# Performance work log

Measured on AMD Instinct MI355X. Metric: run time of the kernel, lower is better.

Reference implementation:

```python
import jax, jax.numpy as jnp
import numpy as np

T, E = 16384, 1024   # frames, feature dim (WavLM-Large)
M, K = 8, 512        # number of kmeans models, clusters per model


def setup_inputs() -> dict:
    key = jax.random.key(0)
    k1, k2, k3 = jax.random.split(key, 3)
    emb = jax.random.normal(k1, (1, T, E), dtype=jnp.float32)
    centroids = jax.random.normal(k2, (M, K, E), dtype=jnp.float32)
    # per-frame random kmeans model choice (stride=1): replaces random.randint in the loop
    model_idx = jax.random.randint(k3, (T,), 0, M, dtype=jnp.int32)
    return {"emb": emb, "centroids": centroids, "model_idx": model_idx}


def reference(emb, centroids, model_idx):
    # emb: [1,T,E], centroids: [M,K,E], model_idx: [T] in [0,M)
    x = emb[0]  # [T,E]
    # squared euclidean distance from every frame to every centroid of every model
    # (argmin over squared dist == argmin over cdist)
    x_sq = jnp.sum(x * x, axis=-1)                      # [T]
    c_sq = jnp.sum(centroids * centroids, axis=-1)      # [M,K]
    dots = jnp.einsum('te,mke->tmk', x, centroids)      # [T,M,K]
    d_all = x_sq[:, None, None] - 2.0 * dots + c_sq[None, :, :]  # [T,M,K]
    # select the randomly chosen model's distances per frame
    d = jnp.take_along_axis(d_all, model_idx[:, None, None].astype(jnp.int32), axis=1)[:, 0, :]  # [T,K]
    codes = jnp.argmin(d, axis=-1)                      # [T]
    # embedding lookup: the quantizer's emb maps cluster id -> centroid vector
    out = centroids[model_idx, codes]                   # [T,E]
    return out[None]  # [1,T,E]
```

## Files before the change

kernel.cpp:

```cpp
#include <hip/hip_runtime.h>


#define T_FRAMES 16384
#define E_DIM    1024
#define M_MODELS 8
#define K_CLUST  512

#define FPB  64
#define NCH  8
#define CHG  16

typedef __bf16 bf16x8 __attribute__((ext_vector_type(8)));
typedef float  floatx16 __attribute__((ext_vector_type(16)));

__device__ __forceinline__ bf16x8 cvt8(const float4 a, const float4 b) {
  bf16x8 h;
  h[0] = (__bf16)a.x; h[1] = (__bf16)a.y; h[2] = (__bf16)a.z; h[3] = (__bf16)a.w;
  h[4] = (__bf16)b.x; h[5] = (__bf16)b.y; h[6] = (__bf16)b.z; h[7] = (__bf16)b.w;
  return h;
}

__global__ __launch_bounds__(256) void k_csq(const float* __restrict__ cent,
                                             double* __restrict__ csq64) {
  const int row = blockIdx.x * 4 + (threadIdx.x >> 6);
  const int lane = threadIdx.x & 63;
  const float* p = cent + (size_t)row * E_DIM;
  double s = 0.0;
#pragma unroll
  for (int i = 0; i < 16; ++i) {
    const float v = p[lane + i * 64];
    s += (double)v * (double)v;
  }
#pragma unroll
  for (int m = 32; m >= 1; m >>= 1) s += __shfl_xor(s, m, 64);
  if (lane == 0) csq64[row] = s;
}

__global__ __launch_bounds__(256) void k_cvt(const float* __restrict__ cent,
                                             float* __restrict__ out) {
  const int b = blockIdx.x;
  const int m = b >> 6;
  const int cg = (b >> 2) & 15;
  const int q = b & 3;
  const int tid = threadIdx.x;
  const int ci = tid & 31;
  const int gk0 = q * 32 + (tid >> 5) * 4;
  const int B32 = (m * 16 + cg) * 32;
  const float* src = cent + ((size_t)(m * K_CLUST + cg * 32 + ci)) * E_DIM;
#pragma unroll
  for (int j = 0; j < 4; ++j) {
    const int gk = gk0 + j;
    const float4 a = *(const float4*)(src + gk * 8);
    const float4 bb = *(const float4*)(src + gk * 8 + 4);
    const size_t foff = (size_t)(B32 + (gk >> 2)) * 1024 + 512 +
                        ((gk & 3) * 32 + ci) * 4;
    *(bf16x8*)(out + foff) = cvt8(a, bb);
  }
}

__global__ __launch_bounds__(256) void k_hist(const int* __restrict__ midx,
                                              int* __restrict__ hist) {
  __shared__ int h[M_MODELS * 33];
  const int tid = threadIdx.x;
  for (int i = tid; i < M_MODELS * 33; i += 256) h[i] = 0;
  __syncthreads();
  const int m = midx[blockIdx.x * 256 + tid];
  atomicAdd(&h[m * 33 + (tid & 31)], 1);
  __syncthreads();
  if (tid < M_MODELS) {
    int s = 0;
    for (int j = 0; j < 32; ++j) s += h[tid * 33 + j];
    hist[blockIdx.x * M_MODELS + tid] = s;
  }
}

__global__ __launch_bounds__(256) void k_scatter(const int* __restrict__ midx,
                                                 const int* __restrict__ hist,
                                                 int* __restrict__ order,
                                                 int* __restrict__ offs) {
  __shared__ int h2[64 * M_MODELS];
  __shared__ int cur[M_MODELS];
  const int tid = threadIdx.x;
  h2[tid] = hist[tid];
  h2[tid + 256] = hist[tid + 256];
  __syncthreads();
  if (tid < M_MODELS) {
    int tot_before = 0;
    for (int mp = 0; mp < tid; ++mp)
      for (int b = 0; b < 64; ++b) tot_before += h2[b * M_MODELS + mp];
    int prior = 0;
    for (int b = 0; b < (int)blockIdx.x; ++b) prior += h2[b * M_MODELS + tid];
    cur[tid] = tot_before + prior;
  }
  if (blockIdx.x == 0 && tid <= M_MODELS) {
    int o = 0;
    for (int mp = 0; mp < tid; ++mp)
      for (int b = 0; b < 64; ++b) o += h2[b * M_MODELS + mp];
    offs[tid] = o;
  }
  __syncthreads();
  const int f = blockIdx.x * 256 + tid;
  const int pos = atomicAdd(&cur[midx[f]], 1);
  order[pos] = f;
}

__global__ __launch_bounds__(256, 1) void k_dist(const float* __restrict__ emb,
                                                 const double* __restrict__ csq64,
                                                 const int* __restrict__ order,
                                                 const int* __restrict__ offs,
                                                 float* __restrict__ out) {
  const int m = blockIdx.x;
  const int o0 = offs[m];
  const int cnt = offs[m + 1] - o0;
  const int start = blockIdx.y * FPB;
  if (start >= cnt) return;
  const int nvalid = min(FPB, cnt - start);

  __shared__ __align__(16) __bf16 A_l[2 * CHG * FPB * 8];

  const int tid = threadIdx.x;
  const int l = tid & 63;
  const int w = tid >> 6;
  const int ln = l & 31;
  const int lh = l >> 5;

  const int s_row = tid >> 2;
  const int s_g = (tid & 3) * 4;
  const size_t arow4 = (size_t)order[o0 + start + min(s_row, nvalid - 1)] * (E_DIM / 4);
  const float4* emb4 = (const float4*)emb;

  float4 pa[8];
#pragma unroll
  for (int j = 0; j < 4; ++j) {
    pa[2 * j] = emb4[arow4 + (s_g + j) * 2];
    pa[2 * j + 1] = emb4[arow4 + (s_g + j) * 2 + 1];
  }
#pragma unroll
  for (int j = 0; j < 4; ++j)
    *(bf16x8*)(A_l + ((size_t)(s_g + j) * FPB + s_row) * 8) = cvt8(pa[2 * j], pa[2 * j + 1]);

  const char* bbase[4];
#pragma unroll
  for (int ct = 0; ct < 4; ++ct) {
    const int cg = w * 4 + ct;
    bbase[ct] = (const char*)out + (size_t)(m * 16 + cg) * 131072 + 2048 + l * 16;
  }
#define LOADB(ct, kb) (*(const bf16x8*)(bbase[ct] + (((kb) >> 1) << 12) + (((kb) & 1) << 10)))

  bf16x8 bR[2][4];
#pragma unroll
  for (int ct = 0; ct < 4; ++ct) {
    bR[0][ct] = LOADB(ct, 0);
    bR[1][ct] = LOADB(ct, 1);
  }

  floatx16 acc[8] = {};
  __syncthreads();

  for (int c = 0; c < NCH; ++c) {
    const int buf = (c & 1) * CHG;
    if (c + 1 < NCH) {
#pragma unroll
      for (int j = 0; j < 4; ++j) {
        pa[2 * j] = emb4[arow4 + (c + 1) * 32 + (s_g + j) * 2];
        pa[2 * j + 1] = emb4[arow4 + (c + 1) * 32 + (s_g + j) * 2 + 1];
      }
    }
#pragma unroll
    for (int jj = 0; jj < 8; ++jj) {
      const int kb = c * 8 + jj;
      const int p = jj & 1;
      const bf16x8 a0 = *(const bf16x8*)(A_l + ((size_t)(buf + jj * 2 + lh) * FPB + ln) * 8);
      const bf16x8 a1 = *(const bf16x8*)(A_l + ((size_t)(buf + jj * 2 + lh) * FPB + 32 + ln) * 8);
#pragma unroll
      for (int ct = 0; ct < 4; ++ct) {
        acc[ct] = __builtin_amdgcn_mfma_f32_32x32x16_bf16(a0, bR[p][ct], acc[ct], 0, 0, 0);
        acc[4 + ct] = __builtin_amdgcn_mfma_f32_32x32x16_bf16(a1, bR[p][ct], acc[4 + ct], 0, 0, 0);
      }
      if (kb + 2 < 64) {
#pragma unroll
        for (int ct = 0; ct < 4; ++ct) bR[p][ct] = LOADB(ct, kb + 2);
      }
    }
    __syncthreads();
    if (c + 1 < NCH) {
      const int nbuf = ((c + 1) & 1) * CHG;
#pragma unroll
      for (int j = 0; j < 4; ++j)
        *(bf16x8*)(A_l + ((size_t)(nbuf + s_g + j) * FPB + s_row) * 8) = cvt8(pa[2 * j], pa[2 * j + 1]);
      __syncthreads();
    }
  }

#pragma unroll
  for (int ct = 0; ct < 4; ++ct) {
    const int col = w * 128 + ct * 32 + ln;
    const float cs = (float)csq64[m * K_CLUST + col];
#pragma unroll
    for (int rt = 0; rt < 2; ++rt) {
#pragma unroll
      for (int r = 0; r < 16; ++r) {
        const int frow = rt * 32 + (r & 3) + 8 * (r >> 2) + 4 * lh;
        const int t = order[o0 + start + min(frow, nvalid - 1)];
        out[(size_t)t * E_DIM + col] = cs - 2.0f * acc[rt * 4 + ct][r];
      }
    }
  }
#undef LOADB
}

__global__ __launch_bounds__(256) void k_pick(const float* __restrict__ emb,
                                              const float* __restrict__ cent,
                                              const double* __restrict__ csq64,
                                              const int* __restrict__ midx,
                                              float* __restrict__ out) {
  const int t = blockIdx.x * 4 + (threadIdx.x >> 6);
  const int l = threadIdx.x & 63;
  const int m = midx[t];

  const float4* orow4 = (const float4*)(out + (size_t)t * E_DIM);
  const float4 v0 = orow4[l * 2];
  const float4 v1 = orow4[l * 2 + 1];
  float sv[8] = {v0.x, v0.y, v0.z, v0.w, v1.x, v1.y, v1.z, v1.w};

  float bm = sv[0];
  int bc = l * 8;
#pragma unroll
  for (int j = 1; j < 8; ++j)
    if (sv[j] < bm) { bm = sv[j]; bc = l * 8 + j; }
#pragma unroll
  for (int s = 32; s >= 1; s >>= 1) {
    const float om = __shfl_xor(bm, s, 64);
    const int oc = __shfl_xor(bc, s, 64);
    if (om < bm || (om == bm && oc < bc)) { bm = om; bc = oc; }
  }

  const float thr = bm + 3.0f;
  unsigned long long bal[8];
  int ncand = 0;
#pragma unroll
  for (int j = 0; j < 8; ++j) {
    bal[j] = __ballot(sv[j] < thr);
    ncand += __popcll(bal[j]);
  }

  int best = bc;
  if (ncand > 1) {
    float4 xv[4];
#pragma unroll
    for (int q = 0; q < 4; ++q)
      xv[q] = *(const float4*)(emb + (size_t)t * E_DIM + q * 256 + l * 4);
    double bd = 1e300;
    int bi = 1 << 30;
#pragma unroll
    for (int j = 0; j < 8; ++j) {
      unsigned long long mb = bal[j];
      while (mb) {
        const int L = __ffsll(mb) - 1;
        mb &= mb - 1;
        const int c = L * 8 + j;
        const float* crow = cent + ((size_t)m * K_CLUST + c) * E_DIM;
        double s = 0.0;
#pragma unroll
        for (int q = 0; q < 4; ++q) {
          const float4 cv = *(const float4*)(crow + q * 256 + l * 4);
          s += (double)xv[q].x * (double)cv.x + (double)xv[q].y * (double)cv.y +
               (double)xv[q].z * (double)cv.z + (double)xv[q].w * (double)cv.w;
        }
#pragma unroll
        for (int sh = 32; sh >= 1; sh >>= 1) s += __shfl_xor(s, sh, 64);
        const double d = csq64[m * K_CLUST + c] - 2.0 * s;
        if (d < bd || (d == bd && c < bi)) { bd = d; bi = c; }
      }
    }
    best = bi;
  }

  const float* crow = cent + ((size_t)m * K_CLUST + best) * E_DIM;
  float* drow = out + (size_t)t * E_DIM;
#pragma unroll
  for (int q = 0; q < 4; ++q)
    *(float4*)(drow + q * 256 + l * 4) = *(const float4*)(crow + q * 256 + l * 4);
}

extern "C" void kernel_launch(void* const* d_in, const int* in_sizes, int n_in,
                              void* d_out, int out_size, void* d_ws, size_t ws_size,
                              hipStream_t stream) {
  const float* emb = (const float*)d_in[0];
  const float* cent = (const float*)d_in[1];
  const int* midx = (const int*)d_in[2];
  float* out = (float*)d_out;

  char* ws = (char*)d_ws;
  double* csq64 = (double*)(ws + 0);
  int* hist = (int*)(ws + 32768);
  int* offs = (int*)(ws + 34816);
  int* order = (int*)(ws + 34880);

  hipLaunchKernelGGL(k_csq, dim3(1024), dim3(256), 0, stream, cent, csq64);
  hipLaunchKernelGGL(k_cvt, dim3(512), dim3(256), 0, stream, cent, out);
  hipLaunchKernelGGL(k_hist, dim3(64), dim3(256), 0, stream, midx, hist);
  hipLaunchKernelGGL(k_scatter, dim3(64), dim3(256), 0, stream, midx, hist, order, offs);
  hipLaunchKernelGGL(k_dist, dim3(M_MODELS, 40), dim3(256), 0, stream,
                     emb, csq64, order, offs, out);
  hipLaunchKernelGGL(k_pick, dim3(T_FRAMES / 4), dim3(256), 0, stream,
                     emb, cent, csq64, midx, out);
}
```

Baseline: 208.6 us.

## Fuse argmin and fp64 candidate refinement into distance kernel, shrink frame tile

The distance GEMM kernel now computes the per-frame argmin directly from MFMA accumulators, using wave shuffles and shared memory. Candidates within the threshold are collected in shared memory and refined in fp64 inside the same kernel. Only an int code per frame is written, so the full fp32 distance matrix no longer makes a round trip through global memory. The frame tile drops from 64 to 32 with two blocks per CU and twice the grid, and a new lightweight gather kernel copies the centroid rows. The risks are halved reuse of each B fragment per frame and the candidate cap of 32 per frame in shared memory.

```diff
diff --git a/kernel.cpp b/kernel.cpp
--- a/kernel.cpp
+++ b/kernel.cpp
@@ -6,9 +6,8 @@
 #define M_MODELS 8
 #define K_CLUST  512
 
-#define FPB  64
-#define NCH  8
-#define CHG  16
+#define FPB 32
+#define NCH 8
 
 typedef __bf16 bf16x8 __attribute__((ext_vector_type(8)));
 typedef float  floatx16 __attribute__((ext_vector_type(16)));
@@ -104,7 +103,8 @@
   order[pos] = f;
 }
 
-__global__ __launch_bounds__(256, 1) void k_dist(const float* __restrict__ emb,
+__global__ __launch_bounds__(256, 2) void k_dist(const float* __restrict__ emb,
+                                                 const float* __restrict__ cent,
                                                  const double* __restrict__ csq64,
                                                  const int* __restrict__ order,
                                                  const int* __restrict__ offs,
@@ -116,7 +116,13 @@
   if (start >= cnt) return;
   const int nvalid = min(FPB, cnt - start);
 
-  __shared__ __align__(16) __bf16 A_l[2 * CHG * FPB * 8];
+  __shared__ __align__(16) __bf16 A_l[2 * 16 * FPB * 8];
+  __shared__ int rows_l[FPB];
+  __shared__ float wmin_s[4][FPB];
+  __shared__ int wcol_s[4][FPB];
+  __shared__ float gmin_s[FPB];
+  __shared__ int cnt_s[FPB];
+  __shared__ int cand_s[FPB][32];
 
   const int tid = threadIdx.x;
   const int l = tid & 63;
@@ -124,20 +130,19 @@
   const int ln = l & 31;
   const int lh = l >> 5;
 
-  const int s_row = tid >> 2;
-  const int s_g = (tid & 3) * 4;
-  const size_t arow4 = (size_t)order[o0 + start + min(s_row, nvalid - 1)] * (E_DIM / 4);
+  if (tid < FPB) rows_l[tid] = order[o0 + start + min(tid, nvalid - 1)];
+  __syncthreads();
+
+  const int s_row = tid & 31;
+  const int s_gp = tid >> 5;
   const float4* emb4 = (const float4*)emb;
-
-  float4 pa[8];
-#pragma unroll
-  for (int j = 0; j < 4; ++j) {
-    pa[2 * j] = emb4[arow4 + (s_g + j) * 2];
-    pa[2 * j + 1] = emb4[arow4 + (s_g + j) * 2 + 1];
-  }
-#pragma unroll
-  for (int j = 0; j < 4; ++j)
-    *(bf16x8*)(A_l + ((size_t)(s_g + j) * FPB + s_row) * 8) = cvt8(pa[2 * j], pa[2 * j + 1]);
+  const size_t arow4 = (size_t)rows_l[s_row] * (E_DIM / 4);
+
+  float4 pa[4];
+#pragma unroll
+  for (int j = 0; j < 4; ++j) pa[j] = emb4[arow4 + s_gp * 4 + j];
+  *(bf16x8*)(A_l + ((s_gp * 2 + 0) * FPB + s_row) * 8) = cvt8(pa[0], pa[1]);
+  *(bf16x8*)(A_l + ((s_gp * 2 + 1) * FPB + s_row) * 8) = cvt8(pa[2], pa[3]);
 
   const char* bbase[4];
 #pragma unroll
@@ -147,140 +152,142 @@
   }
 #define LOADB(ct, kb) (*(const bf16x8*)(bbase[ct] + (((kb) >> 1) << 12) + (((kb) & 1) << 10)))
 
-  bf16x8 bR[2][4];
-#pragma unroll
-  for (int ct = 0; ct < 4; ++ct) {
-    bR[0][ct] = LOADB(ct, 0);
-    bR[1][ct] = LOADB(ct, 1);
-  }
-
-  floatx16 acc[8] = {};
-  __syncthreads();
+  bf16x8 bR[4][4];
+#pragma unroll
+  for (int d = 0; d < 4; ++d)
+#pragma unroll
+    for (int ct = 0; ct < 4; ++ct) bR[d][ct] = LOADB(ct, d);
+
+  floatx16 acc[4] = {};
 
   for (int c = 0; c < NCH; ++c) {
-    const int buf = (c & 1) * CHG;
+    __syncthreads();
+    const int buf = (c & 1) * 16;
     if (c + 1 < NCH) {
 #pragma unroll
-      for (int j = 0; j < 4; ++j) {
-        pa[2 * j] = emb4[arow4 + (c + 1) * 32 + (s_g + j) * 2];
-        pa[2 * j + 1] = emb4[arow4 + (c + 1) * 32 + (s_g + j) * 2 + 1];
-      }
+      for (int j = 0; j < 4; ++j) pa[j] = emb4[arow4 + (c + 1) * 32 + s_gp * 4 + j];
     }
 #pragma unroll
     for (int jj = 0; jj < 8; ++jj) {
       const int kb = c * 8 + jj;
-      const int p = jj & 1;
-      const bf16x8 a0 = *(const bf16x8*)(A_l + ((size_t)(buf + jj * 2 + lh) * FPB + ln) * 8);
-      const bf16x8 a1 = *(const bf16x8*)(A_l + ((size_t)(buf + jj * 2 + lh) * FPB + 32 + ln) * 8);
-#pragma unroll
-      for (int ct = 0; ct < 4; ++ct) {
+      const int p = kb & 3;
+      const bf16x8 a0 = *(const bf16x8*)(A_l + ((buf + jj * 2 + lh) * FPB + ln) * 8);
+#pragma unroll
+      for (int ct = 0; ct < 4; ++ct)
         acc[ct] = __builtin_amdgcn_mfma_f32_32x32x16_bf16(a0, bR[p][ct], acc[ct], 0, 0, 0);
-        acc[4 + ct] = __builtin_amdgcn_mfma_f32_32x32x16_bf16(a1, bR[p][ct], acc[4 + ct], 0, 0, 0);
+      if (kb + 4 < 64) {
+#pragma unroll
+        for (int ct = 0; ct < 4; ++ct) bR[p][ct] = LOADB(ct, kb + 4);
       }
-      if (kb + 2 < 64) {
-#pragma unroll
-        for (int ct = 0; ct < 4; ++ct) bR[p][ct] = LOADB(ct, kb + 2);
+    }
+    if (c + 1 < NCH) {
+      const int nbuf = ((c + 1) & 1) * 16;
+      *(bf16x8*)(A_l + ((nbuf + s_gp * 2 + 0) * FPB + s_row) * 8) = cvt8(pa[0], pa[1]);
+      *(bf16x8*)(A_l + ((nbuf + s_gp * 2 + 1) * FPB + s_row) * 8) = cvt8(pa[2], pa[3]);
+    }
+  }
+#undef LOADB
+
+  float cs[4];
+#pragma unroll
+  for (int ct = 0; ct < 4; ++ct)
+    cs[ct] = (float)csq64[m * K_CLUST + w * 128 + ct * 32 + ln];
+
+#pragma unroll
+  for (int r = 0; r < 16; ++r) {
+    const int fr = (r & 3) + 8 * (r >> 2) + 4 * lh;
+    float bm = cs[0] - 2.0f * acc[0][r];
+    int bc = w * 128 + ln;
+#pragma unroll
+    for (int ct = 1; ct < 4; ++ct) {
+      const float s = cs[ct] - 2.0f * acc[ct][r];
+      if (s < bm) { bm = s; bc = w * 128 + ct * 32 + ln; }
+    }
+#pragma unroll
+    for (int sh = 1; sh <= 16; sh <<= 1) {
+      const float om = __shfl_xor(bm, sh, 64);
+      const int oc = __shfl_xor(bc, sh, 64);
+      if (om < bm || (om == bm && oc < bc)) { bm = om; bc = oc; }
+    }
+    if (ln == 0) { wmin_s[w][fr] = bm; wcol_s[w][fr] = bc; }
+  }
+  __syncthreads();
+
+  if (tid < FPB) {
+    float g = wmin_s[0][tid];
+    int gc = wcol_s[0][tid];
+#pragma unroll
+    for (int w2 = 1; w2 < 4; ++w2) {
+      const float v = wmin_s[w2][tid];
+      const int vc = wcol_s[w2][tid];
+      if (v < g || (v == g && vc < gc)) { g = v; gc = vc; }
+    }
+    gmin_s[tid] = g;
+    cnt_s[tid] = 0;
+  }
+  __syncthreads();
+
+#pragma unroll
+  for (int r = 0; r < 16; ++r) {
+    const int fr = (r & 3) + 8 * (r >> 2) + 4 * lh;
+    const float thr = gmin_s[fr] + 3.0f;
+#pragma unroll
+    for (int ct = 0; ct < 4; ++ct) {
+      const float s = cs[ct] - 2.0f * acc[ct][r];
+      if (s < thr) {
+        const int ix = atomicAdd(&cnt_s[fr], 1);
+        if (ix < 32) cand_s[fr][ix] = w * 128 + ct * 32 + ln;
       }
     }
-    __syncthreads();
-    if (c + 1 < NCH) {
-      const int nbuf = ((c + 1) & 1) * CHG;
-#pragma unroll
-      for (int j = 0; j < 4; ++j)
-        *(bf16x8*)(A_l + ((size_t)(nbuf + s_g + j) * FPB + s_row) * 8) = cvt8(pa[2 * j], pa[2 * j + 1]);
-      __syncthreads();
-    }
-  }
-
-#pragma unroll
-  for (int ct = 0; ct < 4; ++ct) {
-    const int col = w * 128 + ct * 32 + ln;
-    const float cs = (float)csq64[m * K_CLUST + col];
-#pragma unroll
-    for (int rt = 0; rt < 2; ++rt) {
-#pragma unroll
-      for (int r = 0; r < 16; ++r) {
-        const int frow = rt * 32 + (r & 3) + 8 * (r >> 2) + 4 * lh;
-        const int t = order[o0 + start + min(frow, nvalid - 1)];
-        out[(size_t)t * E_DIM + col] = cs - 2.0f * acc[rt * 4 + ct][r];
+  }
+  __syncthreads();
+
+  for (int i = 0; i < 8; ++i) {
+    const int f = w * 8 + i;
+    const int t = rows_l[f];
+    const int n = min(cnt_s[f], 32);
+    int code;
+    if (n == 1) {
+      code = cand_s[f][0];
+    } else {
+      float4 xv[4];
+#pragma unroll
+      for (int q = 0; q < 4; ++q) xv[q] = emb4[(size_t)t * (E_DIM / 4) + q * 64 + l];
+      double bd = 1e300;
+      int bi = 1 << 30;
+      for (int j = 0; j < n; ++j) {
+        const int cc = cand_s[f][j];
+        const float4* crow4 = (const float4*)(cent + ((size_t)(m * K_CLUST + cc)) * E_DIM);
+        double s = 0.0;
+#pragma unroll
+        for (int q = 0; q < 4; ++q) {
+          const float4 cv = crow4[q * 64 + l];
+          s += (double)xv[q].x * cv.x + (double)xv[q].y * cv.y +
+               (double)xv[q].z * cv.z + (double)xv[q].w * cv.w;
+        }
+#pragma unroll
+        for (int sh = 32; sh >= 1; sh >>= 1) s += __shfl_xor(s, sh, 64);
+        const double d = csq64[m * K_CLUST + cc] - 2.0 * s;
+        if (d < bd || (d == bd && cc < bi)) { bd = d; bi = cc; }
       }
-    }
-  }
-#undef LOADB
-}
-
-__global__ __launch_bounds__(256) void k_pick(const float* __restrict__ emb,
-                                              const float* __restrict__ cent,
-                                              const double* __restrict__ csq64,
-                                              const int* __restrict__ midx,
-                                              float* __restrict__ out) {
+      code = bi;
+    }
+    if (l == 0) *(int*)(out + (size_t)t * E_DIM) = code;
+  }
+}
+
+__global__ __launch_bounds__(256) void k_gather(const float* __restrict__ cent,
+                                                const int* __restrict__ midx,
+                                                float* __restrict__ out) {
   const int t = blockIdx.x * 4 + (threadIdx.x >> 6);
   const int l = threadIdx.x & 63;
+  float* drow = out + (size_t)t * E_DIM;
+  const int code = *(const int*)drow;
   const int m = midx[t];
-
-  const float4* orow4 = (const float4*)(out + (size_t)t * E_DIM);
-  const float4 v0 = orow4[l * 2];
-  const float4 v1 = orow4[l * 2 + 1];
-  float sv[8] = {v0.x, v0.y, v0.z, v0.w, v1.x, v1.y, v1.z, v1.w};
-
-  float bm = sv[0];
-  int bc = l * 8;
-#pragma unroll
-  for (int j = 1; j < 8; ++j)
-    if (sv[j] < bm) { bm = sv[j]; bc = l * 8 + j; }
-#pragma unroll
-  for (int s = 32; s >= 1; s >>= 1) {
-    const float om = __shfl_xor(bm, s, 64);
-    const int oc = __shfl_xor(bc, s, 64);
-    if (om < bm || (om == bm && oc < bc)) { bm = om; bc = oc; }
-  }
-
-  const float thr = bm + 3.0f;
-  unsigned long long bal[8];
-  int ncand = 0;
-#pragma unroll
-  for (int j = 0; j < 8; ++j) {
-    bal[j] = __ballot(sv[j] < thr);
-    ncand += __popcll(bal[j]);
-  }
-
-  int best = bc;
-  if (ncand > 1) {
-    float4 xv[4];
-#pragma unroll
-    for (int q = 0; q < 4; ++q)
-      xv[q] = *(const float4*)(emb + (size_t)t * E_DIM + q * 256 + l * 4);
-    double bd = 1e300;
-    int bi = 1 << 30;
-#pragma unroll
-    for (int j = 0; j < 8; ++j) {
-      unsigned long long mb = bal[j];
-      while (mb) {
-        const int L = __ffsll(mb) - 1;
-        mb &= mb - 1;
-        const int c = L * 8 + j;
-        const float* crow = cent + ((size_t)m * K_CLUST + c) * E_DIM;
-        double s = 0.0;
-#pragma unroll
-        for (int q = 0; q < 4; ++q) {
-          const float4 cv = *(const float4*)(crow + q * 256 + l * 4);
-          s += (double)xv[q].x * (double)cv.x + (double)xv[q].y * (double)cv.y +
-               (double)xv[q].z * (double)cv.z + (double)xv[q].w * (double)cv.w;
-        }
-#pragma unroll
-        for (int sh = 32; sh >= 1; sh >>= 1) s += __shfl_xor(s, sh, 64);
-        const double d = csq64[m * K_CLUST + c] - 2.0 * s;
-        if (d < bd || (d == bd && c < bi)) { bd = d; bi = c; }
-      }
-    }
-    best = bi;
-  }
-
-  const float* crow = cent + ((size_t)m * K_CLUST + best) * E_DIM;
-  float* drow = out + (size_t)t * E_DIM;
-#pragma unroll
-  for (int q = 0; q < 4; ++q)
-    *(float4*)(drow + q * 256 + l * 4) = *(const float4*)(crow + q * 256 + l * 4);
+  const float4* src = (const float4*)(cent + ((size_t)(m * K_CLUST + code)) * E_DIM);
+  float4* dst = (float4*)drow;
+#pragma unroll
+  for (int q = 0; q < 4; ++q) dst[q * 64 + l] = src[q * 64 + l];
 }
 
 extern "C" void kernel_launch(void* const* d_in, const int* in_sizes, int n_in,
@@ -297,12 +304,12 @@
   int* offs = (int*)(ws + 34816);
   int* order = (int*)(ws + 34880);
 
+  hipLaunchKernelGGL(k_cvt, dim3(512), dim3(256), 0, stream, cent, out);
   hipLaunchKernelGGL(k_csq, dim3(1024), dim3(256), 0, stream, cent, csq64);
-  hipLaunchKernelGGL(k_cvt, dim3(512), dim3(256), 0, stream, cent, out);
   hipLaunchKernelGGL(k_hist, dim3(64), dim3(256), 0, stream, midx, hist);
   hipLaunchKernelGGL(k_scatter, dim3(64), dim3(256), 0, stream, midx, hist, order, offs);
-  hipLaunchKernelGGL(k_dist, dim3(M_MODELS, 40), dim3(256), 0, stream,
-                     emb, csq64, order, offs, out);
-  hipLaunchKernelGGL(k_pick, dim3(T_FRAMES / 4), dim3(256), 0, stream,
-                     emb, cent, csq64, midx, out);
-}
+  hipLaunchKernelGGL(k_dist, dim3(M_MODELS, 80), dim3(256), 0, stream,
+                     emb, cent, csq64, order, offs, out);
+  hipLaunchKernelGGL(k_gather, dim3(T_FRAMES / 4), dim3(256), 0, stream,
+                     cent, midx, out);
+}
```

Measured after the change: 205.9 us. No clear change (-1.3%).
